# Performance work log

Measured on AMD Instinct MI355X. Metric: run time of the kernel, lower is better.

## Reference

```python
import jax, jax.numpy as jnp
import numpy as np

T, H, F, E, K = 1024, 1024, 2048, 8, 2  # tokens, hidden, ffn_inter, experts, top_k


def setup_inputs() -> dict:
    key = jax.random.key(0)
    ks = jax.random.split(key, 7)
    return {
        "hidden_states": jax.random.normal(ks[0], (T, H), dtype=jnp.float32),
        "token_selected_experts": jax.random.randint(ks[1], (T, K), 0, E, dtype=jnp.int32),
        "token_final_scales": jax.random.uniform(ks[2], (T, K), dtype=jnp.float32),
        "w1": jax.random.normal(ks[3], (E, 2 * F, H), dtype=jnp.float32) * 0.02,  # gated fc1: [gate; linear]
        "b1": jax.random.normal(ks[4], (E, 2 * F), dtype=jnp.float32) * 0.02,
        "w2": jax.random.normal(ks[5], (E, H, F), dtype=jnp.float32) * 0.02,
        "b2": jax.random.normal(ks[6], (E, H), dtype=jnp.float32) * 0.02,
    }


def reference(hidden_states, token_selected_experts, token_final_scales, w1, b1, w2, b2):
    # Grouped GEMM fc1 over all experts: [T, E, 2F]
    h1 = jnp.einsum('th,efh->tef', hidden_states, w1) + b1[None]
    ffn = w2.shape[2]
    gate, lin = h1[..., :ffn], h1[..., ffn:]
    act = jax.nn.silu(gate) * lin                      # swiglu gated activation, [T, E, F]
    y_all = jnp.einsum('tef,ehf->teh', act, w2) + b2[None]  # fc2, [T, E, H]
    # Gather the top-k selected experts per token and combine with final scales
    sel = token_selected_experts.astype(jnp.int32)     # [T, K]
    y_sel = jnp.take_along_axis(y_all, sel[:, :, None], axis=1)  # [T, K, H]
    out = jnp.sum(y_sel * token_final_scales[:, :, None], axis=1)  # [T, H]
    return out
```

## Files before the change

kernel.cpp:

```cpp
#include <hip/hip_runtime.h>
#include <hip/hip_bf16.h>
#include <cstdint>
#include <cstddef>

#define TDIM 1024
#define HDIM 1024
#define FDIM 2048
#define NEXP 8
#define NENT 2048

typedef __bf16 bf16_t;
typedef __bf16 bf16x4 __attribute__((ext_vector_type(4)));
typedef __bf16 bf16x8 __attribute__((ext_vector_type(8)));
typedef float  f32x4  __attribute__((ext_vector_type(4)));

#define WS_COUNTS   0
#define WS_COUNTS2  32
#define WS_OFFSETS  64
#define WS_ETOK     128
#define WS_ESCALE   (WS_ETOK + NENT*4)
#define WS_ACT      (WS_ESCALE + NENT*4)

__global__ void route_count(const int* __restrict__ sel, int* __restrict__ counts) {
  int i = blockIdx.x*256 + threadIdx.x;
  if (i < NENT) atomicAdd(&counts[sel[i]], 1);
}

__global__ void route_scan(const int* __restrict__ counts, int* __restrict__ offsets) {
  if (threadIdx.x == 0) {
    int s = 0;
    for (int e = 0; e < NEXP; e++) { offsets[e] = s; s += counts[e]; }
    offsets[NEXP] = s;
  }
}

__global__ void route_fill(const int* __restrict__ sel, const float* __restrict__ scal,
                           const int* __restrict__ offsets, int* __restrict__ counts2,
                           int* __restrict__ etok, float* __restrict__ escale) {
  int i = blockIdx.x*256 + threadIdx.x;
  if (i < NENT) {
    int e = sel[i];
    int pos = offsets[e] + atomicAdd(&counts2[e], 1);
    etok[pos]   = i >> 1;
    escale[pos] = scal[i];
  }
}

#define BM 64
#define BN 64
#define BK 64
#define LSTR 72
#define KSPLIT2 2

__global__ __launch_bounds__(256, 3) void gemm1_kernel(
    const float* __restrict__ hidden, const float* __restrict__ w1,
    const float* __restrict__ b1, const int* __restrict__ offsets,
    const int* __restrict__ etok, bf16_t* __restrict__ act)
{
  const int e   = blockIdx.z;
  const int off = offsets[e];
  const int nt  = offsets[e+1] - off;
  const int m0  = blockIdx.y * BM;
  if (m0 >= nt) return;
  const int n0  = blockIdx.x * BN;

  __shared__ bf16_t As[BM*LSTR];
  __shared__ bf16_t Bg[BN*LSTR];
  __shared__ bf16_t Bl[BN*LSTR];

  const int tid  = threadIdx.x;
  const int row  = tid >> 2;
  const int seg  = (tid & 3) * 16;

  int aent = m0 + row; if (aent > nt-1) aent = nt-1;
  const int atok = etok[off + aent];
  const float* aptr = hidden + (size_t)atok*HDIM + seg;
  const float* gptr = w1 + ((size_t)e*2*FDIM + (size_t)(n0 + row))*HDIM + seg;
  const float* lptr = gptr + (size_t)FDIM*HDIM;

  const int wave = tid >> 6, lane = tid & 63;
  const int wr = wave >> 1, wc = wave & 1;
  const int quad = lane >> 4, lr = lane & 15;

  float4 a4[4], g4[4], l4[4];
  {
    const float4* p;
    p = (const float4*)aptr; a4[0]=p[0]; a4[1]=p[1]; a4[2]=p[2]; a4[3]=p[3];
    p = (const float4*)gptr; g4[0]=p[0]; g4[1]=p[1]; g4[2]=p[2]; g4[3]=p[3];
    p = (const float4*)lptr; l4[0]=p[0]; l4[1]=p[1]; l4[2]=p[2]; l4[3]=p[3];
  }

  f32x4 accg[2][2] = {};
  f32x4 accl[2][2] = {};

  for (int k0 = 0; k0 < HDIM; k0 += BK) {
    __syncthreads();
    {
      bf16_t* dst = &As[row*LSTR + seg];
      bf16x8 v;
      v[0]=(bf16_t)a4[0].x; v[1]=(bf16_t)a4[0].y; v[2]=(bf16_t)a4[0].z; v[3]=(bf16_t)a4[0].w;
      v[4]=(bf16_t)a4[1].x; v[5]=(bf16_t)a4[1].y; v[6]=(bf16_t)a4[1].z; v[7]=(bf16_t)a4[1].w;
      *(bf16x8*)dst = v;
      v[0]=(bf16_t)a4[2].x; v[1]=(bf16_t)a4[2].y; v[2]=(bf16_t)a4[2].z; v[3]=(bf16_t)a4[2].w;
      v[4]=(bf16_t)a4[3].x; v[5]=(bf16_t)a4[3].y; v[6]=(bf16_t)a4[3].z; v[7]=(bf16_t)a4[3].w;
      *(bf16x8*)(dst+8) = v;
      dst = &Bg[row*LSTR + seg];
      v[0]=(bf16_t)g4[0].x; v[1]=(bf16_t)g4[0].y; v[2]=(bf16_t)g4[0].z; v[3]=(bf16_t)g4[0].w;
      v[4]=(bf16_t)g4[1].x; v[5]=(bf16_t)g4[1].y; v[6]=(bf16_t)g4[1].z; v[7]=(bf16_t)g4[1].w;
      *(bf16x8*)dst = v;
      v[0]=(bf16_t)g4[2].x; v[1]=(bf16_t)g4[2].y; v[2]=(bf16_t)g4[2].z; v[3]=(bf16_t)g4[2].w;
      v[4]=(bf16_t)g4[3].x; v[5]=(bf16_t)g4[3].y; v[6]=(bf16_t)g4[3].z; v[7]=(bf16_t)g4[3].w;
      *(bf16x8*)(dst+8) = v;
      dst = &Bl[row*LSTR + seg];
      v[0]=(bf16_t)l4[0].x; v[1]=(bf16_t)l4[0].y; v[2]=(bf16_t)l4[0].z; v[3]=(bf16_t)l4[0].w;
      v[4]=(bf16_t)l4[1].x; v[5]=(bf16_t)l4[1].y; v[6]=(bf16_t)l4[1].z; v[7]=(bf16_t)l4[1].w;
      *(bf16x8*)dst = v;
      v[0]=(bf16_t)l4[2].x; v[1]=(bf16_t)l4[2].y; v[2]=(bf16_t)l4[2].z; v[3]=(bf16_t)l4[2].w;
      v[4]=(bf16_t)l4[3].x; v[5]=(bf16_t)l4[3].y; v[6]=(bf16_t)l4[3].z; v[7]=(bf16_t)l4[3].w;
      *(bf16x8*)(dst+8) = v;
    }
    __syncthreads();

    if (k0 + BK < HDIM) {
      const float4* p;
      p = (const float4*)(aptr + k0 + BK); a4[0]=p[0]; a4[1]=p[1]; a4[2]=p[2]; a4[3]=p[3];
      p = (const float4*)(gptr + k0 + BK); g4[0]=p[0]; g4[1]=p[1]; g4[2]=p[2]; g4[3]=p[3];
      p = (const float4*)(lptr + k0 + BK); l4[0]=p[0]; l4[1]=p[1]; l4[2]=p[2]; l4[3]=p[3];
    }

    #pragma unroll
    for (int kk = 0; kk < BK; kk += 32) {
      bf16x8 af[2], gf[2], lf[2];
      #pragma unroll
      for (int i = 0; i < 2; i++)
        af[i] = *(const bf16x8*)&As[(wr*32 + i*16 + lr)*LSTR + kk + quad*8];
      #pragma unroll
      for (int j = 0; j < 2; j++) {
        gf[j] = *(const bf16x8*)&Bg[(wc*32 + j*16 + lr)*LSTR + kk + quad*8];
        lf[j] = *(const bf16x8*)&Bl[(wc*32 + j*16 + lr)*LSTR + kk + quad*8];
      }
      #pragma unroll
      for (int i = 0; i < 2; i++)
        #pragma unroll
        for (int j = 0; j < 2; j++) {
          accg[i][j] = __builtin_amdgcn_mfma_f32_16x16x32_bf16(af[i], gf[j], accg[i][j], 0, 0, 0);
          accl[i][j] = __builtin_amdgcn_mfma_f32_16x16x32_bf16(af[i], lf[j], accl[i][j], 0, 0, 0);
        }
    }
  }

  #pragma unroll
  for (int j = 0; j < 2; j++) {
    const int f = n0 + wc*32 + j*16 + lr;
    const float bg_ = b1[e*2*FDIM + f];
    const float bl_ = b1[e*2*FDIM + FDIM + f];
    #pragma unroll
    for (int i = 0; i < 2; i++) {
      #pragma unroll
      for (int r = 0; r < 4; r++) {
        const int m = wr*32 + i*16 + quad*4 + r;
        if (m0 + m < nt) {
          const float g = accg[i][j][r] + bg_;
          const float l = accl[i][j][r] + bl_;
          const float s = g / (1.f + __expf(-g)) * l;
          act[(size_t)(off + m0 + m)*FDIM + f] = (bf16_t)s;
        }
      }
    }
  }
}

__global__ __launch_bounds__(256, 4) void gemm2_kernel(
    const bf16_t* __restrict__ act, const float* __restrict__ w2,
    const float* __restrict__ b2, const int* __restrict__ offsets,
    const int* __restrict__ etok, const float* __restrict__ escale,
    float* __restrict__ out)
{
  const int e   = blockIdx.z;
  const int off = offsets[e];
  const int nt  = offsets[e+1] - off;
  const int m0  = blockIdx.y * BM;
  if (m0 >= nt) return;
  const int n0  = (blockIdx.x >> 1) * BN;
  const int kc  = blockIdx.x & 1;
  const int kbeg = kc * (FDIM / KSPLIT2);
  const int kend = kbeg + FDIM / KSPLIT2;

  __shared__ bf16_t As[BM*LSTR];
  __shared__ bf16_t Bs[BN*LSTR];

  const int tid = threadIdx.x;
  const int row = tid >> 2;
  const int seg = (tid & 3) * 16;

  int aent = m0 + row; if (aent > nt-1) aent = nt-1;
  const bf16_t* aptr = act + (size_t)(off + aent)*FDIM + seg;
  const float*  bptr = w2 + ((size_t)e*HDIM + (size_t)(n0 + row))*FDIM + seg;

  const int wave = tid >> 6, lane = tid & 63;
  const int wr = wave >> 1, wc = wave & 1;
  const int quad = lane >> 4, lr = lane & 15;

  uint4  a0, a1;
  float4 b4[4];
  {
    const uint4* ap = (const uint4*)(aptr + kbeg);
    a0 = ap[0]; a1 = ap[1];
    const float4* bp = (const float4*)(bptr + kbeg);
    b4[0]=bp[0]; b4[1]=bp[1]; b4[2]=bp[2]; b4[3]=bp[3];
  }

  f32x4 acc[2][2] = {};

  for (int k0 = kbeg; k0 < kend; k0 += BK) {
    __syncthreads();
    {
      bf16_t* dst = &As[row*LSTR + seg];
      *(uint4*)dst = a0;
      *(uint4*)(dst+8) = a1;
      dst = &Bs[row*LSTR + seg];
      bf16x8 v;
      v[0]=(bf16_t)b4[0].x; v[1]=(bf16_t)b4[0].y; v[2]=(bf16_t)b4[0].z; v[3]=(bf16_t)b4[0].w;
      v[4]=(bf16_t)b4[1].x; v[5]=(bf16_t)b4[1].y; v[6]=(bf16_t)b4[1].z; v[7]=(bf16_t)b4[1].w;
      *(bf16x8*)dst = v;
      v[0]=(bf16_t)b4[2].x; v[1]=(bf16_t)b4[2].y; v[2]=(bf16_t)b4[2].z; v[3]=(bf16_t)b4[2].w;
      v[4]=(bf16_t)b4[3].x; v[5]=(bf16_t)b4[3].y; v[6]=(bf16_t)b4[3].z; v[7]=(bf16_t)b4[3].w;
      *(bf16x8*)(dst+8) = v;
    }
    __syncthreads();

    if (k0 + BK < kend) {
      const uint4* ap = (const uint4*)(aptr + k0 + BK);
      a0 = ap[0]; a1 = ap[1];
      const float4* bp = (const float4*)(bptr + k0 + BK);
      b4[0]=bp[0]; b4[1]=bp[1]; b4[2]=bp[2]; b4[3]=bp[3];
    }

    #pragma unroll
    for (int kk = 0; kk < BK; kk += 32) {
      bf16x8 af[2], bf[2];
      #pragma unroll
      for (int i = 0; i < 2; i++)
        af[i] = *(const bf16x8*)&As[(wr*32 + i*16 + lr)*LSTR + kk + quad*8];
      #pragma unroll
      for (int j = 0; j < 2; j++)
        bf[j] = *(const bf16x8*)&Bs[(wc*32 + j*16 + lr)*LSTR + kk + quad*8];
      #pragma unroll
      for (int i = 0; i < 2; i++)
        #pragma unroll
        for (int j = 0; j < 2; j++)
          acc[i][j] = __builtin_amdgcn_mfma_f32_16x16x32_bf16(af[i], bf[j], acc[i][j], 0, 0, 0);
    }
  }

  #pragma unroll
  for (int i = 0; i < 2; i++) {
    #pragma unroll
    for (int r = 0; r < 4; r++) {
      const int m = wr*32 + i*16 + quad*4 + r;
      if (m0 + m < nt) {
        const int slot = off + m0 + m;
        const int t    = etok[slot];
        const float s  = escale[slot];
        #pragma unroll
        for (int j = 0; j < 2; j++) {
          const int n = n0 + wc*32 + j*16 + lr;
          float v = acc[i][j][r];
          if (kc == 0) v += b2[e*HDIM + n];
          atomicAdd(&out[(size_t)t*HDIM + n], s * v);
        }
      }
    }
  }
}

extern "C" void kernel_launch(void* const* d_in, const int* in_sizes, int n_in,
                              void* d_out, int out_size, void* d_ws, size_t ws_size,
                              hipStream_t stream) {
  const float* hidden = (const float*)d_in[0];
  const int*   sel    = (const int*)d_in[1];
  const float* scal   = (const float*)d_in[2];
  const float* w1     = (const float*)d_in[3];
  const float* b1     = (const float*)d_in[4];
  const float* w2     = (const float*)d_in[5];
  const float* b2     = (const float*)d_in[6];
  float* out = (float*)d_out;

  char* ws = (char*)d_ws;
  int*    counts  = (int*)(ws + WS_COUNTS);
  int*    counts2 = (int*)(ws + WS_COUNTS2);
  int*    offsets = (int*)(ws + WS_OFFSETS);
  int*    etok    = (int*)(ws + WS_ETOK);
  float*  escale  = (float*)(ws + WS_ESCALE);
  bf16_t* act     = (bf16_t*)(ws + WS_ACT);

  hipMemsetAsync(ws, 0, 64, stream);
  hipMemsetAsync(d_out, 0, (size_t)out_size * sizeof(float), stream);

  route_count<<<NENT/256, 256, 0, stream>>>(sel, counts);
  route_scan <<<1, 64, 0, stream>>>(counts, offsets);
  route_fill <<<NENT/256, 256, 0, stream>>>(sel, scal, offsets, counts2, etok, escale);

  gemm1_kernel<<<dim3(FDIM/BN, NENT/BM, NEXP), 256, 0, stream>>>(hidden, w1, b1, offsets, etok, act);
  gemm2_kernel<<<dim3((HDIM/BN)*KSPLIT2, NENT/BM, NEXP), 256, 0, stream>>>(act, w2, b2, offsets, etok, escale, out);
}
```

Baseline: 361.3 us.

## Pre-convert weights and activations to bf16 and use direct-to-LDS loads in GEMMs

Adds a bulk conversion kernel that turns w1, w2 and hidden states into bf16 copies in the workspace. New grouped GEMM kernels then load these with global_load_lds into XOR-swizzled shared tiles instead of converting fp32 in registers. Routing is merged into one single-block kernel. The conversion adds a large extra write and reread of the weights on every call, and the new path only runs when the workspace is large enough.

```diff
diff --git a/kernel.cpp b/kernel.cpp
--- a/kernel.cpp
+++ b/kernel.cpp
@@ -13,6 +13,19 @@
 typedef __bf16 bf16x4 __attribute__((ext_vector_type(4)));
 typedef __bf16 bf16x8 __attribute__((ext_vector_type(8)));
 typedef float  f32x4  __attribute__((ext_vector_type(4)));
+
+#define W1_ELEMS ((size_t)NEXP*2*FDIM*HDIM)
+#define W2_ELEMS ((size_t)NEXP*HDIM*FDIM)
+#define H_ELEMS  ((size_t)TDIM*HDIM)
+
+#define WB_OFFSETS 0
+#define WB_ETOK    64
+#define WB_ESCALE  (WB_ETOK + NENT*4)
+#define WB_ACT     16512
+#define WB_W1      (WB_ACT + (size_t)NENT*FDIM*2)
+#define WB_W2      (WB_W1 + W1_ELEMS*2)
+#define WB_H       (WB_W2 + W2_ELEMS*2)
+#define WB_END     (WB_H + H_ELEMS*2)
 
 #define WS_COUNTS   0
 #define WS_COUNTS2  32
@@ -21,11 +34,261 @@
 #define WS_ESCALE   (WS_ETOK + NENT*4)
 #define WS_ACT      (WS_ESCALE + NENT*4)
 
+__device__ __forceinline__ void gload16(const void* g, void* l) {
+  __builtin_amdgcn_global_load_lds((const __attribute__((address_space(1))) void*)g,
+                                   (__attribute__((address_space(3))) void*)l, 16, 0, 0);
+}
+
+__global__ void route_all(const int* __restrict__ sel, const float* __restrict__ scal,
+                          int* __restrict__ offsets, int* __restrict__ etok,
+                          float* __restrict__ escale) {
+  __shared__ int cnt[NEXP], cnt2[NEXP], offs[NEXP+1];
+  const int t = threadIdx.x;
+  if (t < NEXP) { cnt[t] = 0; cnt2[t] = 0; }
+  __syncthreads();
+  int e8[8];
+  #pragma unroll
+  for (int q = 0; q < 8; q++) {
+    int i = t*8 + q;
+    e8[q] = sel[i];
+    atomicAdd(&cnt[e8[q]], 1);
+  }
+  __syncthreads();
+  if (t == 0) {
+    int s = 0;
+    for (int e = 0; e < NEXP; e++) { offs[e] = s; offsets[e] = s; s += cnt[e]; }
+    offs[NEXP] = s; offsets[NEXP] = s;
+  }
+  __syncthreads();
+  #pragma unroll
+  for (int q = 0; q < 8; q++) {
+    int i = t*8 + q;
+    int e = e8[q];
+    int pos = offs[e] + atomicAdd(&cnt2[e], 1);
+    etok[pos]   = i >> 1;
+    escale[pos] = scal[i];
+  }
+}
+
+#define CV_GROUPS ((W1_ELEMS + W2_ELEMS + H_ELEMS) / 8)
+__global__ void convert_kernel(const float* __restrict__ w1, const float* __restrict__ w2,
+                               const float* __restrict__ h,
+                               bf16_t* __restrict__ w1bf, bf16_t* __restrict__ w2bf,
+                               bf16_t* __restrict__ hbf) {
+  size_t idx = ((size_t)blockIdx.x*256 + threadIdx.x) * 8;
+  const float* src; bf16_t* dst;
+  if (idx < W1_ELEMS)                { src = w1 + idx;                       dst = w1bf + idx; }
+  else if (idx < W1_ELEMS+W2_ELEMS)  { size_t j = idx - W1_ELEMS;            src = w2 + j; dst = w2bf + j; }
+  else                               { size_t j = idx - W1_ELEMS - W2_ELEMS; src = h  + j; dst = hbf  + j; }
+  float4 v0 = ((const float4*)src)[0];
+  float4 v1 = ((const float4*)src)[1];
+  bf16x8 o;
+  o[0]=(bf16_t)v0.x; o[1]=(bf16_t)v0.y; o[2]=(bf16_t)v0.z; o[3]=(bf16_t)v0.w;
+  o[4]=(bf16_t)v1.x; o[5]=(bf16_t)v1.y; o[6]=(bf16_t)v1.z; o[7]=(bf16_t)v1.w;
+  *(bf16x8*)dst = o;
+}
+
+
+__global__ __launch_bounds__(256, 4) void gemm1_bf(
+    const bf16_t* __restrict__ hbf, const bf16_t* __restrict__ w1bf,
+    const float* __restrict__ b1, const int* __restrict__ offsets,
+    const int* __restrict__ etok, bf16_t* __restrict__ act)
+{
+  const int e   = blockIdx.z;
+  const int off = offsets[e];
+  const int nt  = offsets[e+1] - off;
+  const int m0  = blockIdx.y * 64;
+  if (m0 >= nt) return;
+  const int n0  = blockIdx.x * 64;
+
+  __shared__ __align__(16) bf16_t As[64*64];
+  __shared__ __align__(16) bf16_t Bg[64*64];
+  __shared__ __align__(16) bf16_t Bl[64*64];
+
+  const int tid  = threadIdx.x;
+  const int w    = tid >> 6, lane = tid & 63;
+  const int quad = lane >> 4, lr = lane & 15;
+  const int wr   = w >> 1,  wc = w & 1;
+
+  const int lrow = lane >> 3;
+  const int ssrc = ((lane & 7) ^ lrow) * 8;
+
+  const bf16_t *asrc[2], *gsrc[2], *lsrc[2];
+  bf16_t *adst[2], *gdst[2], *ldst[2];
+  #pragma unroll
+  for (int i = 0; i < 2; i++) {
+    const int r = w*16 + i*8 + lrow;
+    int aent = m0 + r; if (aent > nt-1) aent = nt-1;
+    const int tok = etok[off + aent];
+    asrc[i] = hbf  + (size_t)tok*HDIM + ssrc;
+    gsrc[i] = w1bf + ((size_t)e*2*FDIM + n0 + r)*HDIM + ssrc;
+    lsrc[i] = gsrc[i] + (size_t)FDIM*HDIM;
+    adst[i] = &As[(w*16 + i*8)*64];
+    gdst[i] = &Bg[(w*16 + i*8)*64];
+    ldst[i] = &Bl[(w*16 + i*8)*64];
+  }
+
+  f32x4 accg[2][2] = {}, accl[2][2] = {};
+
+  for (int k0 = 0; k0 < HDIM; k0 += 64) {
+    __syncthreads();
+    #pragma unroll
+    for (int i = 0; i < 2; i++) {
+      gload16(asrc[i] + k0, adst[i]);
+      gload16(gsrc[i] + k0, gdst[i]);
+      gload16(lsrc[i] + k0, ldst[i]);
+    }
+    __syncthreads();
+
+    #pragma unroll
+    for (int kk = 0; kk < 64; kk += 32) {
+      const int g = quad + (kk >> 3);
+      bf16x8 af[2], gf[2], lf[2];
+      #pragma unroll
+      for (int i = 0; i < 2; i++) {
+        const int m = wr*32 + i*16 + lr;
+        af[i] = *(const bf16x8*)&As[m*64 + (g ^ (m & 7))*8];
+      }
+      #pragma unroll
+      for (int j = 0; j < 2; j++) {
+        const int n = wc*32 + j*16 + lr;
+        gf[j] = *(const bf16x8*)&Bg[n*64 + (g ^ (n & 7))*8];
+        lf[j] = *(const bf16x8*)&Bl[n*64 + (g ^ (n & 7))*8];
+      }
+      #pragma unroll
+      for (int i = 0; i < 2; i++)
+        #pragma unroll
+        for (int j = 0; j < 2; j++) {
+          accg[i][j] = __builtin_amdgcn_mfma_f32_16x16x32_bf16(af[i], gf[j], accg[i][j], 0, 0, 0);
+          accl[i][j] = __builtin_amdgcn_mfma_f32_16x16x32_bf16(af[i], lf[j], accl[i][j], 0, 0, 0);
+        }
+    }
+  }
+
+  #pragma unroll
+  for (int j = 0; j < 2; j++) {
+    const int f = n0 + wc*32 + j*16 + lr;
+    const float bg_ = b1[e*2*FDIM + f];
+    const float bl_ = b1[e*2*FDIM + FDIM + f];
+    #pragma unroll
+    for (int i = 0; i < 2; i++) {
+      #pragma unroll
+      for (int r = 0; r < 4; r++) {
+        const int m = wr*32 + i*16 + quad*4 + r;
+        if (m0 + m < nt) {
+          const float g = accg[i][j][r] + bg_;
+          const float l = accl[i][j][r] + bl_;
+          const float s = g / (1.f + __expf(-g)) * l;
+          act[(size_t)(off + m0 + m)*FDIM + f] = (bf16_t)s;
+        }
+      }
+    }
+  }
+}
+
+__global__ __launch_bounds__(256, 4) void gemm2_bf(
+    const bf16_t* __restrict__ act, const bf16_t* __restrict__ w2bf,
+    const float* __restrict__ b2, const int* __restrict__ offsets,
+    const int* __restrict__ etok, const float* __restrict__ escale,
+    float* __restrict__ out)
+{
+  const int e   = blockIdx.z;
+  const int off = offsets[e];
+  const int nt  = offsets[e+1] - off;
+  const int m0  = blockIdx.y * 64;
+  if (m0 >= nt) return;
+  const int n0  = (blockIdx.x >> 1) * 64;
+  const int kc  = blockIdx.x & 1;
+  const int kbeg = kc * (FDIM/2);
+  const int kend = kbeg + FDIM/2;
+
+  __shared__ __align__(16) bf16_t As[64*64];
+  __shared__ __align__(16) bf16_t Bs[64*64];
+
+  const int tid  = threadIdx.x;
+  const int w    = tid >> 6, lane = tid & 63;
+  const int quad = lane >> 4, lr = lane & 15;
+  const int wr   = w >> 1,  wc = w & 1;
+
+  const int lrow = lane >> 3;
+  const int ssrc = ((lane & 7) ^ lrow) * 8;
+
+  const bf16_t *asrc[2], *bsrc[2];
+  bf16_t *adst[2], *bdst[2];
+  #pragma unroll
+  for (int i = 0; i < 2; i++) {
+    const int r = w*16 + i*8 + lrow;
+    int aent = m0 + r; if (aent > nt-1) aent = nt-1;
+    asrc[i] = act  + (size_t)(off + aent)*FDIM + ssrc;
+    bsrc[i] = w2bf + ((size_t)e*HDIM + n0 + r)*FDIM + ssrc;
+    adst[i] = &As[(w*16 + i*8)*64];
+    bdst[i] = &Bs[(w*16 + i*8)*64];
+  }
+
+  f32x4 acc[2][2] = {};
+
+  for (int k0 = kbeg; k0 < kend; k0 += 64) {
+    __syncthreads();
+    #pragma unroll
+    for (int i = 0; i < 2; i++) {
+      gload16(asrc[i] + k0, adst[i]);
+      gload16(bsrc[i] + k0, bdst[i]);
+    }
+    __syncthreads();
+
+    #pragma unroll
+    for (int kk = 0; kk < 64; kk += 32) {
+      const int g = quad + (kk >> 3);
+      bf16x8 af[2], bfr[2];
+      #pragma unroll
+      for (int i = 0; i < 2; i++) {
+        const int m = wr*32 + i*16 + lr;
+        af[i] = *(const bf16x8*)&As[m*64 + (g ^ (m & 7))*8];
+      }
+      #pragma unroll
+      for (int j = 0; j < 2; j++) {
+        const int n = wc*32 + j*16 + lr;
+        bfr[j] = *(const bf16x8*)&Bs[n*64 + (g ^ (n & 7))*8];
+      }
+      #pragma unroll
+      for (int i = 0; i < 2; i++)
+        #pragma unroll
+        for (int j = 0; j < 2; j++)
+          acc[i][j] = __builtin_amdgcn_mfma_f32_16x16x32_bf16(af[i], bfr[j], acc[i][j], 0, 0, 0);
+    }
+  }
+
+  #pragma unroll
+  for (int i = 0; i < 2; i++) {
+    #pragma unroll
+    for (int r = 0; r < 4; r++) {
+      const int m = wr*32 + i*16 + quad*4 + r;
+      if (m0 + m < nt) {
+        const int slot = off + m0 + m;
+        const int t    = etok[slot];
+        const float s  = escale[slot];
+        #pragma unroll
+        for (int j = 0; j < 2; j++) {
+          const int n = n0 + wc*32 + j*16 + lr;
+          float v = acc[i][j][r];
+          if (kc == 0) v += b2[e*HDIM + n];
+          atomicAdd(&out[(size_t)t*HDIM + n], s * v);
+        }
+      }
+    }
+  }
+}
+
+#define BM 64
+#define BN 64
+#define BK 64
+#define LSTR 72
+#define KSPLIT2 2
+
 __global__ void route_count(const int* __restrict__ sel, int* __restrict__ counts) {
   int i = blockIdx.x*256 + threadIdx.x;
   if (i < NENT) atomicAdd(&counts[sel[i]], 1);
 }
-
 __global__ void route_scan(const int* __restrict__ counts, int* __restrict__ offsets) {
   if (threadIdx.x == 0) {
     int s = 0;
@@ -33,7 +296,6 @@
     offsets[NEXP] = s;
   }
 }
-
 __global__ void route_fill(const int* __restrict__ sel, const float* __restrict__ scal,
                            const int* __restrict__ offsets, int* __restrict__ counts2,
                            int* __restrict__ etok, float* __restrict__ escale) {
@@ -45,12 +307,6 @@
     escale[pos] = scal[i];
   }
 }
-
-#define BM 64
-#define BN 64
-#define BK 64
-#define LSTR 72
-#define KSPLIT2 2
 
 __global__ __launch_bounds__(256, 3) void gemm1_kernel(
     const float* __restrict__ hidden, const float* __restrict__ w1,
@@ -238,18 +494,18 @@
 
     #pragma unroll
     for (int kk = 0; kk < BK; kk += 32) {
-      bf16x8 af[2], bf[2];
+      bf16x8 af[2], bfr[2];
       #pragma unroll
       for (int i = 0; i < 2; i++)
         af[i] = *(const bf16x8*)&As[(wr*32 + i*16 + lr)*LSTR + kk + quad*8];
       #pragma unroll
       for (int j = 0; j < 2; j++)
-        bf[j] = *(const bf16x8*)&Bs[(wc*32 + j*16 + lr)*LSTR + kk + quad*8];
+        bfr[j] = *(const bf16x8*)&Bs[(wc*32 + j*16 + lr)*LSTR + kk + quad*8];
       #pragma unroll
       for (int i = 0; i < 2; i++)
         #pragma unroll
         for (int j = 0; j < 2; j++)
-          acc[i][j] = __builtin_amdgcn_mfma_f32_16x16x32_bf16(af[i], bf[j], acc[i][j], 0, 0, 0);
+          acc[i][j] = __builtin_amdgcn_mfma_f32_16x16x32_bf16(af[i], bfr[j], acc[i][j], 0, 0, 0);
     }
   }
 
@@ -287,20 +543,34 @@
   float* out = (float*)d_out;
 
   char* ws = (char*)d_ws;
-  int*    counts  = (int*)(ws + WS_COUNTS);
-  int*    counts2 = (int*)(ws + WS_COUNTS2);
-  int*    offsets = (int*)(ws + WS_OFFSETS);
-  int*    etok    = (int*)(ws + WS_ETOK);
-  float*  escale  = (float*)(ws + WS_ESCALE);
-  bf16_t* act     = (bf16_t*)(ws + WS_ACT);
-
-  hipMemsetAsync(ws, 0, 64, stream);
   hipMemsetAsync(d_out, 0, (size_t)out_size * sizeof(float), stream);
 
-  route_count<<<NENT/256, 256, 0, stream>>>(sel, counts);
-  route_scan <<<1, 64, 0, stream>>>(counts, offsets);
-  route_fill <<<NENT/256, 256, 0, stream>>>(sel, scal, offsets, counts2, etok, escale);
-
-  gemm1_kernel<<<dim3(FDIM/BN, NENT/BM, NEXP), 256, 0, stream>>>(hidden, w1, b1, offsets, etok, act);
-  gemm2_kernel<<<dim3((HDIM/BN)*KSPLIT2, NENT/BM, NEXP), 256, 0, stream>>>(act, w2, b2, offsets, etok, escale, out);
-}
+  if (ws_size >= (size_t)WB_END) {
+    int*    offsets = (int*)(ws + WB_OFFSETS);
+    int*    etok    = (int*)(ws + WB_ETOK);
+    float*  escale  = (float*)(ws + WB_ESCALE);
+    bf16_t* act     = (bf16_t*)(ws + WB_ACT);
+    bf16_t* w1bf    = (bf16_t*)(ws + WB_W1);
+    bf16_t* w2bf    = (bf16_t*)(ws + WB_W2);
+    bf16_t* hbf     = (bf16_t*)(ws + WB_H);
+
+    route_all<<<1, 256, 0, stream>>>(sel, scal, offsets, etok, escale);
+    convert_kernel<<<(int)(CV_GROUPS/256), 256, 0, stream>>>(w1, w2, hidden, w1bf, w2bf, hbf);
+    gemm1_bf<<<dim3(FDIM/64, NENT/64, NEXP), 256, 0, stream>>>(hbf, w1bf, b1, offsets, etok, act);
+    gemm2_bf<<<dim3((HDIM/64)*2, NENT/64, NEXP), 256, 0, stream>>>(act, w2bf, b2, offsets, etok, escale, out);
+  } else {
+    int*    counts  = (int*)(ws + WS_COUNTS);
+    int*    counts2 = (int*)(ws + WS_COUNTS2);
+    int*    offsets = (int*)(ws + WS_OFFSETS);
+    int*    etok    = (int*)(ws + WS_ETOK);
+    float*  escale  = (float*)(ws + WS_ESCALE);
+    bf16_t* act     = (bf16_t*)(ws + WS_ACT);
+
+    hipMemsetAsync(ws, 0, 64, stream);
+    route_count<<<NENT/256, 256, 0, stream>>>(sel, counts);
+    route_scan <<<1, 64, 0, stream>>>(counts, offsets);
+    route_fill <<<NENT/256, 256, 0, stream>>>(sel, scal, offsets, counts2, etok, escale);
+    gemm1_kernel<<<dim3(FDIM/BN, NENT/BM, NEXP), 256, 0, stream>>>(hidden, w1, b1, offsets, etok, act);
+    gemm2_kernel<<<dim3((HDIM/BN)*KSPLIT2, NENT/BM, NEXP), 256, 0, stream>>>(act, w2, b2, offsets, etok, escale, out);
+  }
+}
```

New measurement: 338.0 us. 1.07x faster.
